# Kernel tuning notes

Hardware: AMD Instinct MI355X
Metric: run time of the kernel (lower is better)

## Reference

```python
import jax, jax.numpy as jnp
import numpy as np

INPUT_DIM = 1024
OUTPUT_DIM = 1024
SPLINE_POINTS = 4

def setup_inputs() -> dict:
    key = jax.random.key(0)
    k1, k2 = jax.random.split(key)
    x = jax.random.normal(k1, (4096, INPUT_DIM), dtype=jnp.float32)
    spline_coeffs = jax.random.normal(k2, (OUTPUT_DIM, INPUT_DIM, SPLINE_POINTS, 4), dtype=jnp.float32)
    return {"x": x, "spline_coeffs": spline_coeffs}

def reference(x, spline_coeffs):
    # Per-feature min-max normalization over the batch dim (as in the torch code,
    # where x[:, j].min()/max() are taken over the batch).
    xmin = jnp.min(x, axis=0, keepdims=True)   # [1, D]
    xmax = jnp.max(x, axis=0, keepdims=True)
    xn = (x - xmin) / (xmax - xmin)            # [B, D]

    # The original sums the cubic polynomial over all spline_points, so the
    # effective coefficients are the sum over the spline_points axis.
    c = jnp.sum(spline_coeffs, axis=2)         # [O, D, 4]

    x2 = xn * xn
    x3 = x2 * xn
    # out[b, o] = sum_d c0*x^3 + c1*x^2 + c2*x + c3
    out = (jnp.einsum('bd,od->bo', x3, c[..., 0])
           + jnp.einsum('bd,od->bo', x2, c[..., 1])
           + jnp.einsum('bd,od->bo', xn, c[..., 2])
           + jnp.sum(c[..., 3], axis=1)[None, :])
    return out
```

## Files before the change

kernel.cpp:

```cpp
#include <hip/hip_runtime.h>
#include <hip/hip_bf16.h>
#include <stdint.h>
#include <stddef.h>

typedef __bf16 bf16;
typedef __attribute__((ext_vector_type(4))) __bf16 bf16x4;
typedef __attribute__((ext_vector_type(8))) __bf16 bf16x8;
typedef __attribute__((ext_vector_type(4))) float f32x4;

#define BATCH 4096
#define DIM 1024
#define ODIM 1024
#define K3 3072

#define WS_P      0
#define WS_CB     25165824
#define WS_BIAS   31457280
#define WS_PMIN   31461376
#define WS_PMAX   31723520
#define WS_MINV   31985664
#define WS_SCALE  31989760

#define ASYNC16(g, l)                                                          \
  __builtin_amdgcn_global_load_lds(                                            \
      (__attribute__((address_space(1))) void*)(g),                            \
      (__attribute__((address_space(3))) void*)(l), 16, 0, 0)

__global__ void k_minmax_part(const float* __restrict__ x,
                              float* __restrict__ pmin,
                              float* __restrict__ pmax) {
  int col = blockIdx.x * 256 + threadIdx.x;
  int ch = blockIdx.y;
  const float* p = x + (size_t)ch * 64 * DIM + col;
  float mn = 1e30f, mx = -1e30f;
#pragma unroll 8
  for (int r = 0; r < 64; ++r) {
    float v = p[(size_t)r * DIM];
    mn = fminf(mn, v);
    mx = fmaxf(mx, v);
  }
  pmin[ch * DIM + col] = mn;
  pmax[ch * DIM + col] = mx;
}

__global__ void k_minmax_final(const float* __restrict__ pmin,
                               const float* __restrict__ pmax,
                               float* __restrict__ minv,
                               float* __restrict__ scale) {
  int col = blockIdx.x * 256 + threadIdx.x;
  float mn = 1e30f, mx = -1e30f;
#pragma unroll 8
  for (int ch = 0; ch < 64; ++ch) {
    mn = fminf(mn, pmin[ch * DIM + col]);
    mx = fmaxf(mx, pmax[ch * DIM + col]);
  }
  minv[col] = mn;
  scale[col] = 1.0f / (mx - mn);
}

__global__ void k_prep(const float* __restrict__ x,
                       const float* __restrict__ minv,
                       const float* __restrict__ scale,
                       bf16* __restrict__ P,
                       const float* __restrict__ sp,
                       bf16* __restrict__ CB,
                       float* __restrict__ bias) {
  __shared__ float red[4];
  const int t = threadIdx.x;
  if (blockIdx.x < BATCH) {
    const int b = blockIdx.x;
    const int d = t << 2;
    f32x4 xv = *(const f32x4*)(x + (size_t)b * DIM + d);
    f32x4 mn = *(const f32x4*)(minv + d);
    f32x4 sc = *(const f32x4*)(scale + d);
    bf16x4 o3, o2, o1;
#pragma unroll
    for (int j = 0; j < 4; ++j) {
      float xn = (xv[j] - mn[j]) * sc[j];
      float x2 = xn * xn;
      float x3 = x2 * xn;
      o3[j] = (bf16)x3;
      o2[j] = (bf16)x2;
      o1[j] = (bf16)xn;
    }
    size_t base = (size_t)b * K3 + d;
    *(bf16x4*)(P + base) = o3;
    *(bf16x4*)(P + base + 1024) = o2;
    *(bf16x4*)(P + base + 2048) = o1;
  } else {
    const int o = blockIdx.x - BATCH;
    const int d = t << 2;
    f32x4 s[4];
#pragma unroll
    for (int dd = 0; dd < 4; ++dd) {
      const float* p = sp + ((size_t)o * DIM + d + dd) * 16;
      f32x4 acc = *(const f32x4*)(p);
      acc += *(const f32x4*)(p + 4);
      acc += *(const f32x4*)(p + 8);
      acc += *(const f32x4*)(p + 12);
      s[dd] = acc;
    }
    size_t cb = (size_t)o * K3 + d;
    bf16x4 c0 = {(bf16)s[0][0], (bf16)s[1][0], (bf16)s[2][0], (bf16)s[3][0]};
    bf16x4 c1 = {(bf16)s[0][1], (bf16)s[1][1], (bf16)s[2][1], (bf16)s[3][1]};
    bf16x4 c2 = {(bf16)s[0][2], (bf16)s[1][2], (bf16)s[2][2], (bf16)s[3][2]};
    *(bf16x4*)(CB + cb) = c0;
    *(bf16x4*)(CB + cb + 1024) = c1;
    *(bf16x4*)(CB + cb + 2048) = c2;
    float v = s[0][3] + s[1][3] + s[2][3] + s[3][3];
#pragma unroll
    for (int off = 32; off > 0; off >>= 1) v += __shfl_down(v, off, 64);
    int lane = t & 63, w = t >> 6;
    if (lane == 0) red[w] = v;
    __syncthreads();
    if (t == 0) bias[o] = red[0] + red[1] + red[2] + red[3];
  }
}

#define BM 64
#define BN 128
#define BKE 64
__global__ __launch_bounds__(256, 2) void k_gemm(const bf16* __restrict__ P,
                                                 const bf16* __restrict__ CBm,
                                                 const float* __restrict__ bias,
                                                 float* __restrict__ out) {
  __shared__ bf16 sA[BM * BKE];
  __shared__ bf16 sB[BN * BKE];

  const int tid = threadIdx.x;
  const int wave = tid >> 6;
  const int lane = tid & 63;
  const int bm = blockIdx.x * BM;
  const int bn = blockIdx.y * BN;
  const int wr = (wave >> 1) * 32;
  const int wc = (wave & 1) * 64;

  const char* gA = (const char*)P;
  const char* gB = (const char*)CBm;
  char* lA = (char*)sA;
  char* lB = (char*)sB;
  const size_t rowbytes = (size_t)K3 * 2;

  int srowA[2], sgbA[2];
#pragma unroll
  for (int i = 0; i < 2; ++i) {
    int off = i * 4096 + tid * 16;
    int row = off >> 7;
    int q = (off >> 4) & 7;
    srowA[i] = row;
    sgbA[i] = (q ^ (row & 7)) * 16;
  }
  int srowB[4], sgbB[4];
#pragma unroll
  for (int i = 0; i < 4; ++i) {
    int off = i * 4096 + tid * 16;
    int row = off >> 7;
    int q = (off >> 4) & 7;
    srowB[i] = row;
    sgbB[i] = (q ^ (row & 7)) * 16;
  }

  f32x4 acc[2][4] = {};

  const int mrow = lane & 15;
  const int kq = lane >> 4;

  for (int k0 = 0; k0 < K3; k0 += BKE) {
    const size_t kb = (size_t)k0 * 2;
#pragma unroll
    for (int i = 0; i < 2; ++i)
      ASYNC16(gA + (size_t)(bm + srowA[i]) * rowbytes + kb + sgbA[i],
              lA + i * 4096 + wave * 1024);
#pragma unroll
    for (int i = 0; i < 4; ++i)
      ASYNC16(gB + (size_t)(bn + srowB[i]) * rowbytes + kb + sgbB[i],
              lB + i * 4096 + wave * 1024);
    __syncthreads();

    bf16x8 af[2][2], bg[2][4];
#pragma unroll
    for (int ks = 0; ks < 2; ++ks) {
#pragma unroll
      for (int i = 0; i < 2; ++i) {
        int row = wr + i * 16 + mrow;
        int sq = (ks * 4 + kq) ^ (row & 7);
        af[ks][i] = *(const bf16x8*)&sA[row * BKE + sq * 8];
      }
#pragma unroll
      for (int j = 0; j < 4; ++j) {
        int row = wc + j * 16 + mrow;
        int sq = (ks * 4 + kq) ^ (row & 7);
        bg[ks][j] = *(const bf16x8*)&sB[row * BKE + sq * 8];
      }
    }

#pragma unroll
    for (int ks = 0; ks < 2; ++ks)
#pragma unroll
      for (int i = 0; i < 2; ++i)
#pragma unroll
        for (int j = 0; j < 4; ++j)
          acc[i][j] = __builtin_amdgcn_mfma_f32_16x16x32_bf16(af[ks][i], bg[ks][j],
                                                              acc[i][j], 0, 0, 0);
    __syncthreads();
  }

  const int ccol = lane & 15;
  const int crow = (lane >> 4) * 4;
#pragma unroll
  for (int j = 0; j < 4; ++j) {
    const int col = bn + wc + j * 16 + ccol;
    const float bv = bias[col];
#pragma unroll
    for (int i = 0; i < 2; ++i) {
      const int row0 = bm + wr + i * 16 + crow;
#pragma unroll
      for (int r = 0; r < 4; ++r)
        out[(size_t)(row0 + r) * ODIM + col] = acc[i][j][r] + bv;
    }
  }
}

extern "C" void kernel_launch(void* const* d_in, const int* in_sizes, int n_in,
                              void* d_out, int out_size, void* d_ws, size_t ws_size,
                              hipStream_t stream) {
  (void)in_sizes; (void)n_in; (void)out_size; (void)ws_size;
  const float* x = (const float*)d_in[0];
  const float* sp = (const float*)d_in[1];
  float* out = (float*)d_out;
  char* ws = (char*)d_ws;

  bf16* Pm = (bf16*)(ws + WS_P);
  bf16* CBm = (bf16*)(ws + WS_CB);
  float* bias = (float*)(ws + WS_BIAS);
  float* pmin = (float*)(ws + WS_PMIN);
  float* pmax = (float*)(ws + WS_PMAX);
  float* minv = (float*)(ws + WS_MINV);
  float* scale = (float*)(ws + WS_SCALE);

  k_minmax_part<<<dim3(4, 64), 256, 0, stream>>>(x, pmin, pmax);
  k_minmax_final<<<4, 256, 0, stream>>>(pmin, pmax, minv, scale);
  k_prep<<<BATCH + ODIM, 256, 0, stream>>>(x, minv, scale, Pm, sp, CBm, bias);
  k_gemm<<<dim3(BATCH / BM, ODIM / BN), 256, 0, stream>>>(Pm, CBm, bias, out);
}
```

Measured before the change: 174.7 us.

## Restructure GEMM to 64x64 tiles with 32x32 MFMA and XCD-aware block mapping

The GEMM tile shrinks from 64x128 to 64x64, each wave now computes a single 32x32 block with the 32x32x16 bf16 MFMA, occupancy is raised to 4 blocks per CU, and blocks are remapped to a 1D grid so each XCD handles a contiguous band of rows for L2 locality. The min/max partial reduction now uses 256 chunks of 16 rows with float4 loads and reuses the P workspace region for its partials. The intent is more parallelism and fewer LDS reads per MFMA. The cost is lower arithmetic intensity per block, which doubles global loads of the A operand, and a longer final reduction.

Result: slower. 181.3 us (+3.8%).

```diff
diff --git a/kernel.cpp b/kernel.cpp
--- a/kernel.cpp
+++ b/kernel.cpp
@@ -7,6 +7,7 @@
 typedef __attribute__((ext_vector_type(4))) __bf16 bf16x4;
 typedef __attribute__((ext_vector_type(8))) __bf16 bf16x8;
 typedef __attribute__((ext_vector_type(4))) float f32x4;
+typedef __attribute__((ext_vector_type(16))) float f32x16;
 
 #define BATCH 4096
 #define DIM 1024
@@ -14,12 +15,12 @@
 #define K3 3072
 
 #define WS_P      0
+#define WS_PMIN   0
+#define WS_PMAX   1048576
 #define WS_CB     25165824
 #define WS_BIAS   31457280
-#define WS_PMIN   31461376
-#define WS_PMAX   31723520
-#define WS_MINV   31985664
-#define WS_SCALE  31989760
+#define WS_MINV   31461376
+#define WS_SCALE  31465472
 
 #define ASYNC16(g, l)                                                          \
   __builtin_amdgcn_global_load_lds(                                            \
@@ -29,18 +30,22 @@
 __global__ void k_minmax_part(const float* __restrict__ x,
                               float* __restrict__ pmin,
                               float* __restrict__ pmax) {
-  int col = blockIdx.x * 256 + threadIdx.x;
-  int ch = blockIdx.y;
-  const float* p = x + (size_t)ch * 64 * DIM + col;
-  float mn = 1e30f, mx = -1e30f;
-#pragma unroll 8
-  for (int r = 0; r < 64; ++r) {
-    float v = p[(size_t)r * DIM];
-    mn = fminf(mn, v);
-    mx = fmaxf(mx, v);
-  }
-  pmin[ch * DIM + col] = mn;
-  pmax[ch * DIM + col] = mx;
+  const int t = threadIdx.x;
+  const int ch = blockIdx.x;
+  const float* p = x + (size_t)ch * 16 * DIM + (t << 2);
+  f32x4 mn = {1e30f, 1e30f, 1e30f, 1e30f};
+  f32x4 mx = {-1e30f, -1e30f, -1e30f, -1e30f};
+#pragma unroll
+  for (int r = 0; r < 16; ++r) {
+    f32x4 v = *(const f32x4*)(p + (size_t)r * DIM);
+#pragma unroll
+    for (int j = 0; j < 4; ++j) {
+      mn[j] = fminf(mn[j], v[j]);
+      mx[j] = fmaxf(mx[j], v[j]);
+    }
+  }
+  *(f32x4*)(pmin + ch * DIM + (t << 2)) = mn;
+  *(f32x4*)(pmax + ch * DIM + (t << 2)) = mx;
 }
 
 __global__ void k_minmax_final(const float* __restrict__ pmin,
@@ -50,7 +55,7 @@
   int col = blockIdx.x * 256 + threadIdx.x;
   float mn = 1e30f, mx = -1e30f;
 #pragma unroll 8
-  for (int ch = 0; ch < 64; ++ch) {
+  for (int ch = 0; ch < 256; ++ch) {
     mn = fminf(mn, pmin[ch * DIM + col]);
     mx = fmaxf(mx, pmax[ch * DIM + col]);
   }
@@ -118,9 +123,10 @@
 }
 
 #define BM 64
-#define BN 128
+#define BN 64
 #define BKE 64
-__global__ __launch_bounds__(256, 2) void k_gemm(const bf16* __restrict__ P,
+#define NIT (K3 / BKE)
+__global__ __launch_bounds__(256, 4) void k_gemm(const bf16* __restrict__ P,
                                                  const bf16* __restrict__ CBm,
                                                  const float* __restrict__ bias,
                                                  float* __restrict__ out) {
@@ -130,94 +136,65 @@
   const int tid = threadIdx.x;
   const int wave = tid >> 6;
   const int lane = tid & 63;
-  const int bm = blockIdx.x * BM;
-  const int bn = blockIdx.y * BN;
+
+  const int bid = blockIdx.x;
+  const int xcd = bid & 7;
+  const int local = bid >> 3;
+  const int bm = (xcd * 8 + (local >> 4)) * BM;
+  const int bn = (local & 15) * BN;
+
   const int wr = (wave >> 1) * 32;
-  const int wc = (wave & 1) * 64;
-
-  const char* gA = (const char*)P;
-  const char* gB = (const char*)CBm;
-  char* lA = (char*)sA;
-  char* lB = (char*)sB;
+  const int wc = (wave & 1) * 32;
+
   const size_t rowbytes = (size_t)K3 * 2;
 
-  int srowA[2], sgbA[2];
+  const char* gAp[2];
+  const char* gBp[2];
+  int ldso[2];
 #pragma unroll
   for (int i = 0; i < 2; ++i) {
     int off = i * 4096 + tid * 16;
     int row = off >> 7;
     int q = (off >> 4) & 7;
-    srowA[i] = row;
-    sgbA[i] = (q ^ (row & 7)) * 16;
-  }
-  int srowB[4], sgbB[4];
-#pragma unroll
-  for (int i = 0; i < 4; ++i) {
-    int off = i * 4096 + tid * 16;
-    int row = off >> 7;
-    int q = (off >> 4) & 7;
-    srowB[i] = row;
-    sgbB[i] = (q ^ (row & 7)) * 16;
-  }
-
-  f32x4 acc[2][4] = {};
-
-  const int mrow = lane & 15;
-  const int kq = lane >> 4;
+    int gb = (q ^ (row & 7)) * 16;
+    gAp[i] = (const char*)P + (size_t)(bm + row) * rowbytes + gb;
+    gBp[i] = (const char*)CBm + (size_t)(bn + row) * rowbytes + gb;
+    ldso[i] = i * 4096 + wave * 1024;
+  }
+
+  f32x16 acc = {};
+
+  const int frow = lane & 31;
+  const int fk = lane >> 5;
 
   for (int k0 = 0; k0 < K3; k0 += BKE) {
     const size_t kb = (size_t)k0 * 2;
 #pragma unroll
-    for (int i = 0; i < 2; ++i)
-      ASYNC16(gA + (size_t)(bm + srowA[i]) * rowbytes + kb + sgbA[i],
-              lA + i * 4096 + wave * 1024);
-#pragma unroll
-    for (int i = 0; i < 4; ++i)
-      ASYNC16(gB + (size_t)(bn + srowB[i]) * rowbytes + kb + sgbB[i],
-              lB + i * 4096 + wave * 1024);
+    for (int i = 0; i < 2; ++i) ASYNC16(gAp[i] + kb, (char*)sA + ldso[i]);
+#pragma unroll
+    for (int i = 0; i < 2; ++i) ASYNC16(gBp[i] + kb, (char*)sB + ldso[i]);
     __syncthreads();
 
-    bf16x8 af[2][2], bg[2][4];
-#pragma unroll
-    for (int ks = 0; ks < 2; ++ks) {
-#pragma unroll
-      for (int i = 0; i < 2; ++i) {
-        int row = wr + i * 16 + mrow;
-        int sq = (ks * 4 + kq) ^ (row & 7);
-        af[ks][i] = *(const bf16x8*)&sA[row * BKE + sq * 8];
-      }
-#pragma unroll
-      for (int j = 0; j < 4; ++j) {
-        int row = wc + j * 16 + mrow;
-        int sq = (ks * 4 + kq) ^ (row & 7);
-        bg[ks][j] = *(const bf16x8*)&sB[row * BKE + sq * 8];
-      }
-    }
-
-#pragma unroll
-    for (int ks = 0; ks < 2; ++ks)
-#pragma unroll
-      for (int i = 0; i < 2; ++i)
-#pragma unroll
-        for (int j = 0; j < 4; ++j)
-          acc[i][j] = __builtin_amdgcn_mfma_f32_16x16x32_bf16(af[ks][i], bg[ks][j],
-                                                              acc[i][j], 0, 0, 0);
+#pragma unroll
+    for (int ks = 0; ks < 4; ++ks) {
+      int ra = wr + frow;
+      int ua = (ks * 2 + fk) ^ (ra & 7);
+      bf16x8 af = *(const bf16x8*)&sA[ra * BKE + ua * 8];
+      int rb = wc + frow;
+      int ub = (ks * 2 + fk) ^ (rb & 7);
+      bf16x8 bg = *(const bf16x8*)&sB[rb * BKE + ub * 8];
+      acc = __builtin_amdgcn_mfma_f32_32x32x16_bf16(af, bg, acc, 0, 0, 0);
+    }
     __syncthreads();
   }
 
-  const int ccol = lane & 15;
-  const int crow = (lane >> 4) * 4;
-#pragma unroll
-  for (int j = 0; j < 4; ++j) {
-    const int col = bn + wc + j * 16 + ccol;
-    const float bv = bias[col];
-#pragma unroll
-    for (int i = 0; i < 2; ++i) {
-      const int row0 = bm + wr + i * 16 + crow;
-#pragma unroll
-      for (int r = 0; r < 4; ++r)
-        out[(size_t)(row0 + r) * ODIM + col] = acc[i][j][r] + bv;
-    }
+  const int col = bn + wc + (lane & 31);
+  const float bv = bias[col];
+  const int rbase = bm + wr + 4 * (lane >> 5);
+#pragma unroll
+  for (int r = 0; r < 16; ++r) {
+    int row = rbase + (r & 3) + 8 * (r >> 2);
+    out[(size_t)row * ODIM + col] = acc[r] + bv;
   }
 }
 
@@ -238,8 +215,8 @@
   float* minv = (float*)(ws + WS_MINV);
   float* scale = (float*)(ws + WS_SCALE);
 
-  k_minmax_part<<<dim3(4, 64), 256, 0, stream>>>(x, pmin, pmax);
+  k_minmax_part<<<256, 256, 0, stream>>>(x, pmin, pmax);
   k_minmax_final<<<4, 256, 0, stream>>>(pmin, pmax, minv, scale);
   k_prep<<<BATCH + ODIM, 256, 0, stream>>>(x, minv, scale, Pm, sp, CBm, bias);
-  k_gemm<<<dim3(BATCH / BM, ODIM / BN), 256, 0, stream>>>(Pm, CBm, bias, out);
-}
+  k_gemm<<<1024, 256, 0, stream>>>(Pm, CBm, bias, out);
+}
```
